# Performance work log

Hardware: AMD Instinct MI355X
Metric: run time of the kernel (lower is better)

## Reference

```python
import jax, jax.numpy as jnp
import numpy as np

TOTAL_WORDS = 10000
EMBED_LEN = 100
SEQ_LEN = 80
UNITS = 512
BATCH = 1024


def gru_layer(x_seq, Wx, Wh, b):
    """Keras GRU (reset_after=True), x_seq: [T, B, D] -> ys: [T, B, U]."""
    bi, br = b[0], b[1]  # input bias, recurrent bias, each [3U]
    U = Wh.shape[0]

    def step(h, x_t):
        gx = x_t @ Wx + bi            # [B, 3U]
        gh = h @ Wh + br              # [B, 3U]
        xz, xr, xh = gx[:, :U], gx[:, U:2 * U], gx[:, 2 * U:]
        hz, hr, hn = gh[:, :U], gh[:, U:2 * U], gh[:, 2 * U:]
        z = jax.nn.sigmoid(xz + hz)
        r = jax.nn.sigmoid(xr + hr)
        hh = jnp.tanh(xh + r * hn)
        h_new = z * h + (1.0 - z) * hh
        return h_new, h_new

    h0 = jnp.zeros((x_seq.shape[1], U), dtype=x_seq.dtype)
    _, ys = jax.lax.scan(step, h0, x_seq)
    return ys


def setup_inputs() -> dict:
    key = jax.random.key(0)
    ks = jax.random.split(key, 10)
    tokens = jax.random.randint(ks[0], (BATCH, SEQ_LEN), 0, TOTAL_WORDS, dtype=jnp.int32)
    s_e = 1.0 / np.sqrt(EMBED_LEN)
    s_u = 1.0 / np.sqrt(UNITS)
    emb = jax.random.normal(ks[1], (TOTAL_WORDS, EMBED_LEN), jnp.float32) * 0.05
    Wx1 = jax.random.normal(ks[2], (EMBED_LEN, 3 * UNITS), jnp.float32) * s_e
    Wh1 = jax.random.normal(ks[3], (UNITS, 3 * UNITS), jnp.float32) * s_u
    b1 = jnp.zeros((2, 3 * UNITS), jnp.float32)
    Wx2 = jax.random.normal(ks[4], (UNITS, 3 * UNITS), jnp.float32) * s_u
    Wh2 = jax.random.normal(ks[5], (UNITS, 3 * UNITS), jnp.float32) * s_u
    b2 = jnp.zeros((2, 3 * UNITS), jnp.float32)
    Wfc = jax.random.normal(ks[6], (UNITS, 1), jnp.float32) * s_u
    bfc = jnp.zeros((1,), jnp.float32)
    return {"tokens": tokens, "emb": emb, "Wx1": Wx1, "Wh1": Wh1, "b1": b1,
            "Wx2": Wx2, "Wh2": Wh2, "b2": b2, "Wfc": Wfc, "bfc": bfc}


def reference(tokens, emb, Wx1, Wh1, b1, Wx2, Wh2, b2, Wfc, bfc):
    x = emb[tokens]                       # [B, T, E]
    x = jnp.transpose(x, (1, 0, 2))       # [T, B, E] (scan over time)
    ys1 = gru_layer(x, Wx1, Wh1, b1)      # [T, B, U] return_sequences
    ys2 = gru_layer(ys1, Wx2, Wh2, b2)    # [T, B, U]
    h_last = ys2[-1]                      # [B, U] (last timestep only)
    logits = h_last @ Wfc + bfc           # [B, 1]
    return jax.nn.sigmoid(logits)
```

## Files before the change

### kernel.cpp

```cpp
#include <hip/hip_runtime.h>
#include <hip/hip_bf16.h>
#include <math.h>

typedef float f32x4 __attribute__((ext_vector_type(4)));
typedef int   ix4  __attribute__((ext_vector_type(4)));

#define MFMAI8(a,b,c) __builtin_amdgcn_mfma_i32_16x16x64_i8(a,b,c,0,0,0)

constexpr int BATCH = 1024, SEQ = 80, EMB = 100, U = 512;
constexpr int KC1 = 10;
constexpr int KC2 = 16;
constexpr float EMBMAX = 0.32f;
constexpr float INV127SQ = 1.f / 16129.f;

__device__ __forceinline__ float sigf_(float x) {
  return __builtin_amdgcn_rcpf(1.f + __expf(-x));
}
__device__ __forceinline__ float tanhf_(float x) {
  return fmaf(2.f, __builtin_amdgcn_rcpf(1.f + __expf(-2.f * x)), -1.f);
}

__global__ void k_colmax(const float* __restrict__ Wh1, const float* __restrict__ Wx1,
                         const float* __restrict__ Wh2, const float* __restrict__ Wx2,
                         float* __restrict__ scales) {
  int idx = blockIdx.x * 256 + threadIdx.x;
  if (idx >= 4 * 8 * 1536) return;
  int col = idx % 1536;
  int rest = idx / 1536;
  int kseg = rest & 7, m = rest >> 3;
  const float* W = (m == 0) ? Wh1 : (m == 1) ? Wx1 : (m == 2) ? Wh2 : Wx2;
  int Klim = (m == 1) ? EMB : 512;
  int k0 = kseg * 64, k1 = min(k0 + 64, Klim);
  float mx = 0.f;
  for (int k = k0; k < k1; ++k) mx = fmaxf(mx, fabsf(W[(size_t)k * 1536 + col]));
  if (k1 > k0) atomicMax((int*)&scales[m * 1536 + col], __float_as_int(mx));
}

__device__ __forceinline__ void pack_one(const float* __restrict__ WH,
                                         const float* __restrict__ WX,
                                         const float* __restrict__ scH,
                                         const float* __restrict__ scX,
                                         signed char* __restrict__ out,
                                         int KCH, int KCX, int KXr, int c) {
  int KC = KCH + KCX;
  int lane = c & 63;
  int rest = c >> 6;
  int g = rest % 3; rest /= 3;
  int kc = rest % KC;
  int u16 = rest / KC;
  int col = g * 512 + u16 * 16 + (lane & 15);
  int kl = (lane >> 4) * 16;
  float sH = 127.f / fmaxf(scH[col], 1e-12f);
  float sX = 127.f / fmaxf(scX[col], 1e-12f);
  ix4 v;
  signed char* vb = (signed char*)&v;
#pragma unroll
  for (int e = 0; e < 16; ++e) {
    int q = 0;
    if (kc < KCH) {
      int k = kc * 64 + kl + e;
      q = (int)rintf(WH[(size_t)k * 1536 + col] * sH);
    } else {
      int kx = (kc - KCH) * 64 + kl + e;
      if (kx < KXr) q = (int)rintf(WX[(size_t)kx * 1536 + col] * sX);
    }
    vb[e] = (signed char)q;
  }
  *(ix4*)(out + (size_t)c * 16) = v;
}

__global__ void k_prep(const float* __restrict__ Wh1, const float* __restrict__ Wx1,
                       const float* __restrict__ Wh2, const float* __restrict__ Wx2,
                       const float* __restrict__ scales,
                       signed char* __restrict__ wf1, signed char* __restrict__ wf2,
                       const float* __restrict__ emb, signed char* __restrict__ embq) {
  int b = blockIdx.x, tid = threadIdx.x;
  if (b < 240) {
    int c = b * 256 + tid;
    if (c < 61440) pack_one(Wh1, Wx1, scales, scales + 1536, wf1, 8, 2, EMB, c);
  } else if (b < 624) {
    int c = (b - 240) * 256 + tid;
    if (c < 98304) pack_one(Wh2, Wx2, scales + 3072, scales + 4608, wf2, 8, 8, U, c);
  } else {
    int idx = (b - 624) * 256 + tid;
    if (idx < 320000) {
      int r = idx >> 5, c4 = (idx & 31) * 4;
      char q[4];
#pragma unroll
      for (int j = 0; j < 4; ++j) {
        int c = c4 + j, v = 0;
        if (c < EMB) {
          float x = emb[r * EMB + c] * (127.f / EMBMAX);
          v = (int)rintf(fminf(127.f, fmaxf(-127.f, x)));
        }
        q[j] = (char)v;
      }
      *(int*)(embq + (size_t)r * 128 + c4) = *(int*)q;
    }
  }
}


__device__ __forceinline__ unsigned llc_read(const unsigned* p) {
  unsigned v;
  asm volatile("global_load_dword %0, %1, off sc0 sc1\n\ts_waitcnt vmcnt(0)"
               : "=v"(v) : "v"(p) : "memory");
  return v;
}

__global__ __launch_bounds__(512, 2)
void k_gru_persist(const int* __restrict__ tokens, const signed char* __restrict__ embq,
                   const signed char* __restrict__ wf1, const signed char* __restrict__ wf2,
                   const float* __restrict__ b1, const float* __restrict__ b2,
                   const float* __restrict__ scales,
                   signed char* __restrict__ h1b0, signed char* __restrict__ h1b1,
                   signed char* __restrict__ h2b0, signed char* __restrict__ h2b1,
                   const float* __restrict__ Wfc, const float* __restrict__ bfc,
                   float* __restrict__ out, unsigned* __restrict__ bar) {
  __shared__ __attribute__((aligned(16))) signed char wt2[2 * KC2 * 3 * 1024];
  __shared__ unsigned char s_x[256];
  __shared__ int s_gl;

  const int bid = blockIdx.x, tid = threadIdx.x;
  const int g = bid & 15, lb = bid >> 4;
  const int r0 = g * 64;
  unsigned* fl  = bar + (size_t)g * 16 * 32;
  unsigned* own = fl + (size_t)lb * 32;

  {
    ix4* hz = (ix4*)(h1b0 + (size_t)bid * 8192);
    hz[tid] = (ix4){0, 0, 0, 0};
  }

  unsigned* xslot = bar + 8192;
  unsigned* gcnt  = bar + 8512;
  unsigned xcc = 0;
  asm volatile("s_getreg_b32 %0, hwreg(HW_REG_XCC_ID)" : "=s"(xcc));
  if (tid == 0)
    __hip_atomic_store(&xslot[bid], xcc + 1u, __ATOMIC_RELAXED, __HIP_MEMORY_SCOPE_AGENT);

  __syncthreads();
  if (tid == 0) {
    __builtin_amdgcn_fence(__ATOMIC_RELEASE, "agent");
    __hip_atomic_fetch_add(gcnt, 1u, __ATOMIC_RELAXED, __HIP_MEMORY_SCOPE_AGENT);
    int spin = 0;
    while (__hip_atomic_load(gcnt, __ATOMIC_RELAXED, __HIP_MEMORY_SCOPE_AGENT) < 256u) {
      __builtin_amdgcn_s_sleep(8);
      if (++spin > (1 << 24)) break;
    }
    __builtin_amdgcn_fence(__ATOMIC_ACQUIRE, "agent");
  }
  __syncthreads();

  if (tid < 256)
    s_x[tid] = (unsigned char)__hip_atomic_load(&xslot[tid], __ATOMIC_RELAXED,
                                                __HIP_MEMORY_SCOPE_AGENT);
  __syncthreads();
  if (tid == 0) {
    unsigned char x0 = s_x[g];
    int f = (x0 != 0);
    for (int j = 1; j < 16; ++j) f &= (s_x[g + 16 * j] == x0);
    s_gl = f;
  }
  __syncthreads();
  const bool fastbar = (s_gl != 0);

  {
    const ix4* s2 = (const ix4*)(wf2 + (size_t)lb * 6144 * 16);
    ix4* d2 = (ix4*)wt2;
    for (int i = tid; i < 6144; i += 512) d2[i] = s2[i];
  }

  const int wv = tid >> 6, lane = tid & 63, ln = lane & 15, quad = lane >> 4;
  const int rt = wv >> 1, uh = wv & 1;
  const int u16 = lb * 2 + uh;
  const int rw0 = r0 + rt * 16;
  const int kq = quad * 16;

  ix4 w1[30];
  {
    const ix4* s1 = (const ix4*)(wf1 + (size_t)u16 * KC1 * 3 * 1024);
#pragma unroll
    for (int f = 0; f < 30; ++f) w1[f] = s1[f * 64 + lane];
  }
  const signed char* wt2h = wt2 + uh * (KC2 * 3 * 1024) + lane * 16;

  const int u = u16 * 16 + ln;
  const float* sc_h1 = scales, *sc_x1 = scales + 1536, *sc_h2 = scales + 3072, *sc_x2 = scales + 4608;
  const float fz1h = sc_h1[u] * INV127SQ,        fz1x = sc_x1[u] * (EMBMAX * INV127SQ);
  const float fr1h = sc_h1[512 + u] * INV127SQ,  fr1x = sc_x1[512 + u] * (EMBMAX * INV127SQ);
  const float fn1h = sc_h1[1024 + u] * INV127SQ, fn1x = sc_x1[1024 + u] * (EMBMAX * INV127SQ);
  const float fz2h = sc_h2[u] * INV127SQ,        fz2x = sc_x2[u] * INV127SQ;
  const float fr2h = sc_h2[512 + u] * INV127SQ,  fr2x = sc_x2[512 + u] * INV127SQ;
  const float fn2h = sc_h2[1024 + u] * INV127SQ, fn2x = sc_x2[1024 + u] * INV127SQ;
  const float bz1 = b1[u] + b1[1536 + u],       br1 = b1[512 + u] + b1[2048 + u];
  const float bn1x = b1[1024 + u],              bn1h = b1[2560 + u];
  const float bz2 = b2[u] + b2[1536 + u],       br2 = b2[512 + u] + b2[2048 + u];
  const float bn2x = b2[1024 + u],              bn2h = b2[2560 + u];
  const size_t wb8 = (size_t)(u >> 6) * 65536 + (u & 63);

  float h1st[4] = {0.f, 0.f, 0.f, 0.f};
  float h2st[4] = {0.f, 0.f, 0.f, 0.f};

#pragma unroll 1
  for (int s = 0; s <= SEQ; ++s) {
    const signed char* h1r = (s & 1) ? h1b0 : h1b1;
    signed char*       h1w = (s & 1) ? h1b1 : h1b0;
    const signed char* h2r = (s & 1) ? h2b1 : h2b0;
    signed char*       h2w = (s & 1) ? h2b0 : h2b1;

    ix4 z1h, z1x, r1h, r1x, n1h, n1x, z2h, z2x, r2h, r2x, n2h, n2x;
    z1h = z1x = r1h = r1x = n1h = n1x = (ix4){0, 0, 0, 0};
    z2h = z2x = r2h = r2x = n2h = n2x = (ix4){0, 0, 0, 0};

#pragma unroll
    for (int kc = 0; kc < 8; ++kc) {
      ix4 a = *(const ix4*)(h1r + (size_t)kc * 65536 + (rw0 + ln) * 64 + kq);
      z1h = MFMAI8(a, w1[kc * 3 + 0], z1h);
      r1h = MFMAI8(a, w1[kc * 3 + 1], r1h);
      n1h = MFMAI8(a, w1[kc * 3 + 2], n1h);
      z2x = MFMAI8(a, *(const ix4*)(wt2h + ((8 + kc) * 3 + 0) * 1024), z2x);
      r2x = MFMAI8(a, *(const ix4*)(wt2h + ((8 + kc) * 3 + 1) * 1024), r2x);
      n2x = MFMAI8(a, *(const ix4*)(wt2h + ((8 + kc) * 3 + 2) * 1024), n2x);
    }
#pragma unroll
    for (int kc = 0; kc < 8; ++kc) {
      ix4 a = *(const ix4*)(h2r + (size_t)kc * 65536 + (rw0 + ln) * 64 + kq);
      z2h = MFMAI8(a, *(const ix4*)(wt2h + (kc * 3 + 0) * 1024), z2h);
      r2h = MFMAI8(a, *(const ix4*)(wt2h + (kc * 3 + 1) * 1024), r2h);
      n2h = MFMAI8(a, *(const ix4*)(wt2h + (kc * 3 + 2) * 1024), n2h);
    }
    {
      int se = (s < SEQ) ? s : SEQ - 1;
      int tok = tokens[(size_t)(rw0 + ln) * SEQ + se];
#pragma unroll
      for (int kc = 0; kc < 2; ++kc) {
        ix4 a = *(const ix4*)(embq + (size_t)tok * 128 + kc * 64 + kq);
        z1x = MFMAI8(a, w1[(8 + kc) * 3 + 0], z1x);
        r1x = MFMAI8(a, w1[(8 + kc) * 3 + 1], r1x);
        n1x = MFMAI8(a, w1[(8 + kc) * 3 + 2], n1x);
      }
    }

    if (s < SEQ) {
#pragma unroll
      for (int i = 0; i < 4; ++i) {
        int row = rw0 + quad * 4 + i;
        float z = sigf_(fmaf(fz1h, (float)z1h[i], fmaf(fz1x, (float)z1x[i], bz1)));
        float r = sigf_(fmaf(fr1h, (float)r1h[i], fmaf(fr1x, (float)r1x[i], br1)));
        float hh = tanhf_(fmaf(fn1x, (float)n1x[i], bn1x) +
                          r * fmaf(fn1h, (float)n1h[i], bn1h));
        float hn = hh + z * (h1st[i] - hh);
        h1st[i] = hn;
        h1w[wb8 + (size_t)row * 64] = (signed char)(int)rintf(hn * 127.f);
      }
    }
    if (s >= 1) {
#pragma unroll
      for (int i = 0; i < 4; ++i) {
        int row = rw0 + quad * 4 + i;
        float z = sigf_(fmaf(fz2h, (float)z2h[i], fmaf(fz2x, (float)z2x[i], bz2)));
        float r = sigf_(fmaf(fr2h, (float)r2h[i], fmaf(fr2x, (float)r2x[i], br2)));
        float hh = tanhf_(fmaf(fn2x, (float)n2x[i], bn2x) +
                          r * fmaf(fn2h, (float)n2h[i], bn2h));
        float hn = hh + z * (h2st[i] - hh);
        h2st[i] = hn;
        h2w[wb8 + (size_t)row * 64] = (signed char)(int)rintf(hn * 127.f);
      }
    }

    asm volatile("s_waitcnt vmcnt(0)" ::: "memory");
    __syncthreads();
    if (tid == 0) {
      if (!fastbar) __builtin_amdgcn_fence(__ATOMIC_RELEASE, "agent");
      __hip_atomic_fetch_add(own, 1u, __ATOMIC_RELAXED, __HIP_MEMORY_SCOPE_AGENT);
    }
    if (wv == 0) {
      const unsigned* fp = fl + (size_t)(lane & 15) * 32;
      const unsigned tgt = (unsigned)s + 1u;
      int spin = 0;
      for (;;) {
        unsigned v = llc_read(fp);
        if (__all(v >= tgt)) break;
        __builtin_amdgcn_s_sleep(1);
        if (++spin > (1 << 22)) break;
      }
      if (lane == 0) {
        if (fastbar) {
          asm volatile("buffer_inv sc0\n\ts_waitcnt vmcnt(0)" ::: "memory");
        } else {
          __builtin_amdgcn_fence(__ATOMIC_ACQUIRE, "agent");
        }
      }
    }
    __syncthreads();
  }

  if (wv < 4) {
    int row = r0 + lb * 4 + wv;
    float sfc = 0.f;
#pragma unroll
    for (int j = 0; j < 8; ++j) {
      int k = j * 64 + lane;
      sfc += (float)h2b1[(size_t)j * 65536 + row * 64 + lane] * Wfc[k];
    }
#pragma unroll
    for (int off = 32; off; off >>= 1) sfc += __shfl_down(sfc, off, 64);
    if (lane == 0) out[row] = sigf_(sfc * (1.f / 127.f) + bfc[0]);
  }
}

extern "C" void kernel_launch(void* const* d_in, const int* in_sizes, int n_in,
                              void* d_out, int out_size, void* d_ws, size_t ws_size,
                              hipStream_t stream) {
  const int*   tokens = (const int*)d_in[0];
  const float* emb = (const float*)d_in[1];
  const float* Wx1 = (const float*)d_in[2];
  const float* Wh1 = (const float*)d_in[3];
  const float* b1  = (const float*)d_in[4];
  const float* Wx2 = (const float*)d_in[5];
  const float* Wh2 = (const float*)d_in[6];
  const float* b2  = (const float*)d_in[7];
  const float* Wfc = (const float*)d_in[8];
  const float* bfc = (const float*)d_in[9];
  float* out = (float*)d_out;

  signed char* wf1  = (signed char*)d_ws;
  signed char* wf2  = wf1 + 983040;
  signed char* embq = wf2 + 1572864;
  float* scales     = (float*)(embq + 1280000);
  unsigned* bar     = (unsigned*)((signed char*)scales + 24576);
  signed char* h1b0 = (signed char*)bar + 36864;
  signed char* h1b1 = h1b0 + 524288;
  signed char* h2b0 = h1b1 + 524288;
  signed char* h2b1 = h2b0 + 524288;

  hipMemsetAsync(scales, 0, 24576 + 36864, stream);

  k_colmax<<<(4 * 8 * 1536 + 255) / 256, 256, 0, stream>>>(Wh1, Wx1, Wh2, Wx2, scales);
  k_prep<<<1874, 256, 0, stream>>>(Wh1, Wx1, Wh2, Wx2, scales, wf1, wf2, emb, embq);

  void* args[] = {(void*)&tokens, (void*)&embq, (void*)&wf1, (void*)&wf2,
                  (void*)&b1, (void*)&b2, (void*)&scales,
                  (void*)&h1b0, (void*)&h1b1, (void*)&h2b0, (void*)&h2b1,
                  (void*)&Wfc, (void*)&bfc, (void*)&out, (void*)&bar};
  hipLaunchCooperativeKernel((void*)k_gru_persist, dim3(256), dim3(512), args, 0, stream);
}
```

Baseline: 585.4 us.

## Stage hidden-state tiles into LDS via async loads and use a counter barrier

Each step, the block's 64-row slices of h1 and most of h2 are copied into shared memory with global_load_lds, instead of every wave reading them from global memory separately. The embedding-input MFMAs move ahead of the wait so they overlap the async copies. The 16 per-block flags polled by a whole wave are replaced by one shared counter per group, polled by a single thread. This raises LDS use, which may affect occupancy, and puts all blocks of a group on one contended atomic.

```diff
diff --git a/kernel.cpp b/kernel.cpp
--- a/kernel.cpp
+++ b/kernel.cpp
@@ -12,6 +12,11 @@
 constexpr int KC2 = 16;
 constexpr float EMBMAX = 0.32f;
 constexpr float INV127SQ = 1.f / 16129.f;
+
+constexpr int WT2SZ = 2 * KC2 * 3 * 1024;
+constexpr int A1OFF = WT2SZ;
+constexpr int A2OFF = WT2SZ + 32768;
+constexpr int SMEMSZ = A2OFF + 7 * 4096;
 
 __device__ __forceinline__ float sigf_(float x) {
   return __builtin_amdgcn_rcpf(1.f + __expf(-x));
@@ -100,12 +105,31 @@
   }
 }
 
-
 __device__ __forceinline__ unsigned llc_read(const unsigned* p) {
   unsigned v;
   asm volatile("global_load_dword %0, %1, off sc0 sc1\n\ts_waitcnt vmcnt(0)"
                : "=v"(v) : "v"(p) : "memory");
   return v;
+}
+
+__device__ __forceinline__ void bar_step(unsigned* cnt, unsigned tgt, bool fast) {
+  asm volatile("s_waitcnt vmcnt(0)" ::: "memory");
+  __syncthreads();
+  if (threadIdx.x == 0) {
+    if (!fast) __builtin_amdgcn_fence(__ATOMIC_RELEASE, "agent");
+    __hip_atomic_fetch_add(cnt, 1u, __ATOMIC_RELAXED, __HIP_MEMORY_SCOPE_AGENT);
+    int spin = 0;
+    while (llc_read(cnt) < tgt) {
+      __builtin_amdgcn_s_sleep(1);
+      if (++spin > (1 << 22)) break;
+    }
+    if (fast) {
+      asm volatile("buffer_inv sc0\n\ts_waitcnt vmcnt(0)" ::: "memory");
+    } else {
+      __builtin_amdgcn_fence(__ATOMIC_ACQUIRE, "agent");
+    }
+  }
+  __syncthreads();
 }
 
 __global__ __launch_bounds__(512, 2)
@@ -117,23 +141,20 @@
                    signed char* __restrict__ h2b0, signed char* __restrict__ h2b1,
                    const float* __restrict__ Wfc, const float* __restrict__ bfc,
                    float* __restrict__ out, unsigned* __restrict__ bar) {
-  __shared__ __attribute__((aligned(16))) signed char wt2[2 * KC2 * 3 * 1024];
-  __shared__ unsigned char s_x[256];
-  __shared__ int s_gl;
+  __shared__ __attribute__((aligned(16))) signed char smem[SMEMSZ];
 
   const int bid = blockIdx.x, tid = threadIdx.x;
   const int g = bid & 15, lb = bid >> 4;
   const int r0 = g * 64;
-  unsigned* fl  = bar + (size_t)g * 16 * 32;
-  unsigned* own = fl + (size_t)lb * 32;
+  unsigned* cnt = bar + g * 64;
 
   {
     ix4* hz = (ix4*)(h1b0 + (size_t)bid * 8192);
     hz[tid] = (ix4){0, 0, 0, 0};
   }
 
-  unsigned* xslot = bar + 8192;
-  unsigned* gcnt  = bar + 8512;
+  unsigned* xslot = bar + 1024;
+  unsigned* gcnt  = bar + 1536;
   unsigned xcc = 0;
   asm volatile("s_getreg_b32 %0, hwreg(HW_REG_XCC_ID)" : "=s"(xcc));
   if (tid == 0)
@@ -152,6 +173,8 @@
   }
   __syncthreads();
 
+  unsigned char* s_x = (unsigned char*)&smem[A1OFF];
+  int* s_gl = (int*)&smem[A2OFF];
   if (tid < 256)
     s_x[tid] = (unsigned char)__hip_atomic_load(&xslot[tid], __ATOMIC_RELAXED,
                                                 __HIP_MEMORY_SCOPE_AGENT);
@@ -160,22 +183,25 @@
     unsigned char x0 = s_x[g];
     int f = (x0 != 0);
     for (int j = 1; j < 16; ++j) f &= (s_x[g + 16 * j] == x0);
-    s_gl = f;
-  }
-  __syncthreads();
-  const bool fastbar = (s_gl != 0);
+    *s_gl = f;
+  }
+  __syncthreads();
+  const bool fastbar = (*s_gl != 0);
+  __syncthreads();
 
   {
     const ix4* s2 = (const ix4*)(wf2 + (size_t)lb * 6144 * 16);
-    ix4* d2 = (ix4*)wt2;
+    ix4* d2 = (ix4*)smem;
     for (int i = tid; i < 6144; i += 512) d2[i] = s2[i];
   }
+  __syncthreads();
 
   const int wv = tid >> 6, lane = tid & 63, ln = lane & 15, quad = lane >> 4;
   const int rt = wv >> 1, uh = wv & 1;
   const int u16 = lb * 2 + uh;
   const int rw0 = r0 + rt * 16;
   const int kq = quad * 16;
+  const int lrow64 = (rt * 16 + ln) * 64;
 
   ix4 w1[30];
   {
@@ -183,7 +209,7 @@
 #pragma unroll
     for (int f = 0; f < 30; ++f) w1[f] = s1[f * 64 + lane];
   }
-  const signed char* wt2h = wt2 + uh * (KC2 * 3 * 1024) + lane * 16;
+  const signed char* wt2h = smem + uh * (KC2 * 3 * 1024) + lane * 16;
 
   const int u = u16 * 16 + ln;
   const float* sc_h1 = scales, *sc_x1 = scales + 1536, *sc_h2 = scales + 3072, *sc_x2 = scales + 4608;
@@ -201,6 +227,7 @@
 
   float h1st[4] = {0.f, 0.f, 0.f, 0.f};
   float h2st[4] = {0.f, 0.f, 0.f, 0.f};
+  unsigned tgt = 16u;
 
 #pragma unroll 1
   for (int s = 0; s <= SEQ; ++s) {
@@ -209,13 +236,46 @@
     const signed char* h2r = (s & 1) ? h2b1 : h2b0;
     signed char*       h2w = (s & 1) ? h2b0 : h2b1;
 
+    {
+      const signed char* g1 = h1r + (size_t)wv * 65536 + r0 * 64;
+#pragma unroll
+      for (int i = 0; i < 4; ++i)
+        __builtin_amdgcn_global_load_lds((const int*)(g1 + i * 1024 + lane * 16),
+                                         (int*)&smem[A1OFF + wv * 4096 + i * 1024],
+                                         16, 0, 0);
+      if (wv < 7) {
+        const signed char* g2 = h2r + (size_t)wv * 65536 + r0 * 64;
+#pragma unroll
+        for (int i = 0; i < 4; ++i)
+          __builtin_amdgcn_global_load_lds((const int*)(g2 + i * 1024 + lane * 16),
+                                           (int*)&smem[A2OFF + wv * 4096 + i * 1024],
+                                           16, 0, 0);
+      }
+    }
+    ix4 a27 = *(const ix4*)(h2r + (size_t)7 * 65536 + (rw0 + ln) * 64 + kq);
+
     ix4 z1h, z1x, r1h, r1x, n1h, n1x, z2h, z2x, r2h, r2x, n2h, n2x;
     z1h = z1x = r1h = r1x = n1h = n1x = (ix4){0, 0, 0, 0};
     z2h = z2x = r2h = r2x = n2h = n2x = (ix4){0, 0, 0, 0};
 
+    {
+      int se = (s < SEQ) ? s : SEQ - 1;
+      int tok = tokens[(size_t)(rw0 + ln) * SEQ + se];
+#pragma unroll
+      for (int kc = 0; kc < 2; ++kc) {
+        ix4 a = *(const ix4*)(embq + (size_t)tok * 128 + kc * 64 + kq);
+        z1x = MFMAI8(a, w1[(8 + kc) * 3 + 0], z1x);
+        r1x = MFMAI8(a, w1[(8 + kc) * 3 + 1], r1x);
+        n1x = MFMAI8(a, w1[(8 + kc) * 3 + 2], n1x);
+      }
+    }
+
+    asm volatile("s_waitcnt vmcnt(0)" ::: "memory");
+    __syncthreads();
+
 #pragma unroll
     for (int kc = 0; kc < 8; ++kc) {
-      ix4 a = *(const ix4*)(h1r + (size_t)kc * 65536 + (rw0 + ln) * 64 + kq);
+      ix4 a = *(const ix4*)&smem[A1OFF + kc * 4096 + lrow64 + kq];
       z1h = MFMAI8(a, w1[kc * 3 + 0], z1h);
       r1h = MFMAI8(a, w1[kc * 3 + 1], r1h);
       n1h = MFMAI8(a, w1[kc * 3 + 2], n1h);
@@ -224,23 +284,15 @@
       n2x = MFMAI8(a, *(const ix4*)(wt2h + ((8 + kc) * 3 + 2) * 1024), n2x);
     }
 #pragma unroll
-    for (int kc = 0; kc < 8; ++kc) {
-      ix4 a = *(const ix4*)(h2r + (size_t)kc * 65536 + (rw0 + ln) * 64 + kq);
+    for (int kc = 0; kc < 7; ++kc) {
+      ix4 a = *(const ix4*)&smem[A2OFF + kc * 4096 + lrow64 + kq];
       z2h = MFMAI8(a, *(const ix4*)(wt2h + (kc * 3 + 0) * 1024), z2h);
       r2h = MFMAI8(a, *(const ix4*)(wt2h + (kc * 3 + 1) * 1024), r2h);
       n2h = MFMAI8(a, *(const ix4*)(wt2h + (kc * 3 + 2) * 1024), n2h);
     }
-    {
-      int se = (s < SEQ) ? s : SEQ - 1;
-      int tok = tokens[(size_t)(rw0 + ln) * SEQ + se];
-#pragma unroll
-      for (int kc = 0; kc < 2; ++kc) {
-        ix4 a = *(const ix4*)(embq + (size_t)tok * 128 + kc * 64 + kq);
-        z1x = MFMAI8(a, w1[(8 + kc) * 3 + 0], z1x);
-        r1x = MFMAI8(a, w1[(8 + kc) * 3 + 1], r1x);
-        n1x = MFMAI8(a, w1[(8 + kc) * 3 + 2], n1x);
-      }
-    }
+    z2h = MFMAI8(a27, *(const ix4*)(wt2h + (7 * 3 + 0) * 1024), z2h);
+    r2h = MFMAI8(a27, *(const ix4*)(wt2h + (7 * 3 + 1) * 1024), r2h);
+    n2h = MFMAI8(a27, *(const ix4*)(wt2h + (7 * 3 + 2) * 1024), n2h);
 
     if (s < SEQ) {
 #pragma unroll
@@ -269,31 +321,8 @@
       }
     }
 
-    asm volatile("s_waitcnt vmcnt(0)" ::: "memory");
-    __syncthreads();
-    if (tid == 0) {
-      if (!fastbar) __builtin_amdgcn_fence(__ATOMIC_RELEASE, "agent");
-      __hip_atomic_fetch_add(own, 1u, __ATOMIC_RELAXED, __HIP_MEMORY_SCOPE_AGENT);
-    }
-    if (wv == 0) {
-      const unsigned* fp = fl + (size_t)(lane & 15) * 32;
-      const unsigned tgt = (unsigned)s + 1u;
-      int spin = 0;
-      for (;;) {
-        unsigned v = llc_read(fp);
-        if (__all(v >= tgt)) break;
-        __builtin_amdgcn_s_sleep(1);
-        if (++spin > (1 << 22)) break;
-      }
-      if (lane == 0) {
-        if (fastbar) {
-          asm volatile("buffer_inv sc0\n\ts_waitcnt vmcnt(0)" ::: "memory");
-        } else {
-          __builtin_amdgcn_fence(__ATOMIC_ACQUIRE, "agent");
-        }
-      }
-    }
-    __syncthreads();
+    bar_step(cnt, tgt, fastbar);
+    tgt += 16u;
   }
 
   if (wv < 4) {
@@ -330,12 +359,12 @@
   signed char* embq = wf2 + 1572864;
   float* scales     = (float*)(embq + 1280000);
   unsigned* bar     = (unsigned*)((signed char*)scales + 24576);
-  signed char* h1b0 = (signed char*)bar + 36864;
+  signed char* h1b0 = (signed char*)bar + 8192;
   signed char* h1b1 = h1b0 + 524288;
   signed char* h2b0 = h1b1 + 524288;
   signed char* h2b1 = h2b0 + 524288;
 
-  hipMemsetAsync(scales, 0, 24576 + 36864, stream);
+  hipMemsetAsync(scales, 0, 24576 + 8192, stream);
 
   k_colmax<<<(4 * 8 * 1536 + 255) / 256, 256, 0, stream>>>(Wh1, Wx1, Wh2, Wx2, scales);
   k_prep<<<1874, 256, 0, stream>>>(Wh1, Wx1, Wh2, Wx2, scales, wf1, wf2, emb, embq);
```

New measurement: 561.9 us. 1.04x faster.

## Split each block into two independent half-block groups with counter barriers

Applied to the files above, without the earlier changes.

Remaps work so each block owns one 16-unit slice for two 64-row batch groups, with each half of the block (4 waves) synchronizing independently. Block-wide __syncthreads and per-block flag polling are replaced by LDS counters plus a single agent-scope atomic counter per group that one wave polls. The second half starts after a short sleep so the two halves' barrier phases are staggered. Shared weight storage is halved because both halves use the same unit slice. This aims to cut barrier latency and let one half compute while the other waits, at the cost of more complex LDS spin synchronization and contention on a shared global counter.

```diff
diff --git a/kernel.cpp b/kernel.cpp
--- a/kernel.cpp
+++ b/kernel.cpp
@@ -100,7 +100,6 @@
   }
 }
 
-
 __device__ __forceinline__ unsigned llc_read(const unsigned* p) {
   unsigned v;
   asm volatile("global_load_dword %0, %1, off sc0 sc1\n\ts_waitcnt vmcnt(0)"
@@ -117,27 +116,26 @@
                    signed char* __restrict__ h2b0, signed char* __restrict__ h2b1,
                    const float* __restrict__ Wfc, const float* __restrict__ bfc,
                    float* __restrict__ out, unsigned* __restrict__ bar) {
-  __shared__ __attribute__((aligned(16))) signed char wt2[2 * KC2 * 3 * 1024];
+  __shared__ __attribute__((aligned(16))) signed char wt2[KC2 * 3 * 1024];
   __shared__ unsigned char s_x[256];
   __shared__ int s_gl;
+  __shared__ unsigned scnt[2], srel[2];
 
   const int bid = blockIdx.x, tid = threadIdx.x;
-  const int g = bid & 15, lb = bid >> 4;
-  const int r0 = g * 64;
-  unsigned* fl  = bar + (size_t)g * 16 * 32;
-  unsigned* own = fl + (size_t)lb * 32;
+  const int lb = bid >> 3;
 
   {
     ix4* hz = (ix4*)(h1b0 + (size_t)bid * 8192);
     hz[tid] = (ix4){0, 0, 0, 0};
   }
 
-  unsigned* xslot = bar + 8192;
-  unsigned* gcnt  = bar + 8512;
+  unsigned* xslot = bar + 1024;
+  unsigned* gcnt  = bar + 1536;
   unsigned xcc = 0;
   asm volatile("s_getreg_b32 %0, hwreg(HW_REG_XCC_ID)" : "=s"(xcc));
   if (tid == 0)
     __hip_atomic_store(&xslot[bid], xcc + 1u, __ATOMIC_RELAXED, __HIP_MEMORY_SCOPE_AGENT);
+  if (tid < 2) { scnt[tid] = 0u; srel[tid] = 0u; }
 
   __syncthreads();
   if (tid == 0) {
@@ -157,25 +155,29 @@
                                                 __HIP_MEMORY_SCOPE_AGENT);
   __syncthreads();
   if (tid == 0) {
-    unsigned char x0 = s_x[g];
+    unsigned char x0 = s_x[bid & 7];
     int f = (x0 != 0);
-    for (int j = 1; j < 16; ++j) f &= (s_x[g + 16 * j] == x0);
+    for (int j = 1; j < 32; ++j) f &= (s_x[(bid & 7) + 8 * j] == x0);
     s_gl = f;
   }
   __syncthreads();
   const bool fastbar = (s_gl != 0);
 
   {
-    const ix4* s2 = (const ix4*)(wf2 + (size_t)lb * 6144 * 16);
+    const ix4* s2 = (const ix4*)(wf2 + (size_t)lb * 49152);
     ix4* d2 = (ix4*)wt2;
-    for (int i = tid; i < 6144; i += 512) d2[i] = s2[i];
-  }
+    for (int i = tid; i < 3072; i += 512) d2[i] = s2[i];
+  }
+  __syncthreads();
 
   const int wv = tid >> 6, lane = tid & 63, ln = lane & 15, quad = lane >> 4;
-  const int rt = wv >> 1, uh = wv & 1;
-  const int u16 = lb * 2 + uh;
-  const int rw0 = r0 + rt * 16;
+  const int sub = wv >> 2, wvs = wv & 3;
+  const int g = (bid & 7) * 2 + sub;
+  const int u16 = lb;
+  const int r0 = g * 64;
+  const int rw0 = r0 + wvs * 16;
   const int kq = quad * 16;
+  unsigned* cnt = bar + g * 64;
 
   ix4 w1[30];
   {
@@ -183,7 +185,7 @@
 #pragma unroll
     for (int f = 0; f < 30; ++f) w1[f] = s1[f * 64 + lane];
   }
-  const signed char* wt2h = wt2 + uh * (KC2 * 3 * 1024) + lane * 16;
+  const signed char* wt2h = wt2 + lane * 16;
 
   const int u = u16 * 16 + ln;
   const float* sc_h1 = scales, *sc_x1 = scales + 1536, *sc_h2 = scales + 3072, *sc_x2 = scales + 4608;
@@ -202,6 +204,11 @@
   float h1st[4] = {0.f, 0.f, 0.f, 0.f};
   float h2st[4] = {0.f, 0.f, 0.f, 0.f};
 
+  if (sub) {
+#pragma unroll 1
+    for (int i = 0; i < 12; ++i) __builtin_amdgcn_s_sleep(8);
+  }
+
 #pragma unroll 1
   for (int s = 0; s <= SEQ; ++s) {
     const signed char* h1r = (s & 1) ? h1b0 : h1b1;
@@ -270,34 +277,48 @@
     }
 
     asm volatile("s_waitcnt vmcnt(0)" ::: "memory");
-    __syncthreads();
-    if (tid == 0) {
-      if (!fastbar) __builtin_amdgcn_fence(__ATOMIC_RELEASE, "agent");
-      __hip_atomic_fetch_add(own, 1u, __ATOMIC_RELAXED, __HIP_MEMORY_SCOPE_AGENT);
-    }
-    if (wv == 0) {
-      const unsigned* fp = fl + (size_t)(lane & 15) * 32;
-      const unsigned tgt = (unsigned)s + 1u;
+    if (lane == 0)
+      __hip_atomic_fetch_add(&scnt[sub], 1u, __ATOMIC_RELEASE, __HIP_MEMORY_SCOPE_WORKGROUP);
+    if (wv == (sub << 2) && lane == 0) {
+      unsigned ltgt = 4u * (unsigned)(s + 1);
       int spin = 0;
-      for (;;) {
-        unsigned v = llc_read(fp);
-        if (__all(v >= tgt)) break;
+      while (__hip_atomic_load(&scnt[sub], __ATOMIC_ACQUIRE,
+                               __HIP_MEMORY_SCOPE_WORKGROUP) < ltgt) {
         __builtin_amdgcn_s_sleep(1);
         if (++spin > (1 << 22)) break;
       }
-      if (lane == 0) {
-        if (fastbar) {
-          asm volatile("buffer_inv sc0\n\ts_waitcnt vmcnt(0)" ::: "memory");
-        } else {
-          __builtin_amdgcn_fence(__ATOMIC_ACQUIRE, "agent");
-        }
-      }
-    }
-    __syncthreads();
-  }
+      if (!fastbar) __builtin_amdgcn_fence(__ATOMIC_RELEASE, "agent");
+      __hip_atomic_fetch_add(cnt, 1u, __ATOMIC_RELAXED, __HIP_MEMORY_SCOPE_AGENT);
+      unsigned gtgt = 32u * (unsigned)(s + 1);
+      spin = 0;
+      while (llc_read(cnt) < gtgt) {
+        __builtin_amdgcn_s_sleep(1);
+        if (++spin > (1 << 22)) break;
+      }
+      if (fastbar) {
+        asm volatile("buffer_inv sc0\n\ts_waitcnt vmcnt(0)" ::: "memory");
+      } else {
+        __builtin_amdgcn_fence(__ATOMIC_ACQUIRE, "agent");
+      }
+      __hip_atomic_store(&srel[sub], (unsigned)(s + 1), __ATOMIC_RELEASE,
+                         __HIP_MEMORY_SCOPE_WORKGROUP);
+    }
+    {
+      int spin = 0;
+      while (__hip_atomic_load(&srel[sub], __ATOMIC_ACQUIRE,
+                               __HIP_MEMORY_SCOPE_WORKGROUP) < (unsigned)(s + 1)) {
+        __builtin_amdgcn_s_sleep(1);
+        if (++spin > (1 << 22)) break;
+      }
+      __builtin_amdgcn_sched_barrier(0);
+    }
+  }
+
+  __syncthreads();
 
   if (wv < 4) {
-    int row = r0 + lb * 4 + wv;
+    int grow = (bid & 7) * 2 + (wv >> 1);
+    int row = grow * 64 + lb * 2 + (wv & 1);
     float sfc = 0.f;
 #pragma unroll
     for (int j = 0; j < 8; ++j) {
@@ -330,12 +351,12 @@
   signed char* embq = wf2 + 1572864;
   float* scales     = (float*)(embq + 1280000);
   unsigned* bar     = (unsigned*)((signed char*)scales + 24576);
-  signed char* h1b0 = (signed char*)bar + 36864;
+  signed char* h1b0 = (signed char*)bar + 8192;
   signed char* h1b1 = h1b0 + 524288;
   signed char* h2b0 = h1b1 + 524288;
   signed char* h2b1 = h2b0 + 524288;
 
-  hipMemsetAsync(scales, 0, 24576 + 36864, stream);
+  hipMemsetAsync(scales, 0, 24576 + 8192, stream);
 
   k_colmax<<<(4 * 8 * 1536 + 255) / 256, 256, 0, stream>>>(Wh1, Wx1, Wh2, Wx2, scales);
   k_prep<<<1874, 256, 0, stream>>>(Wh1, Wx1, Wh2, Wx2, scales, wf1, wf2, emb, embq);
```

Result: slower. 744.8 us (+27.2%).
